# Kernel tuning notes

Measured on AMD Instinct MI355X. Metric: run time of the kernel, lower is better.

## Reference

```python
import jax, jax.numpy as jnp
import numpy as np

N_NODES = 100000


def gcn_conv(x, row, col, norm, W, b):
    # PyG GCNConv: linear transform first, then normalized aggregation.
    h = x @ W                                   # [N, D_out]
    msg = h[col] * norm[:, None]                # gather sources, scale  [E', D_out]
    out = jax.ops.segment_sum(msg, row, num_segments=N_NODES)
    return out + b


def _build_norm(edge_index, n):
    # add self-loops
    loops = jnp.arange(n, dtype=edge_index.dtype)
    row = jnp.concatenate([edge_index[0], loops])  # targets
    col = jnp.concatenate([edge_index[1], loops])  # sources
    deg = jax.ops.segment_sum(jnp.ones(row.shape[0], jnp.float32), row, num_segments=n)
    dinv = jnp.where(deg > 0, jax.lax.rsqrt(deg), 0.0)
    norm = dinv[row] * dinv[col]
    return row, col, norm


def setup_inputs() -> dict:
    key = jax.random.key(0)
    k = jax.random.split(key, 5)
    N, E, IN, H, OUT = N_NODES, 1_600_000, 128, 64, 64
    x = jax.random.normal(k[0], (N, IN), jnp.float32)
    edge_index = jax.random.randint(k[1], (2, E), 0, N, dtype=jnp.int32)
    W1 = jax.random.normal(k[2], (IN, H), jnp.float32) / np.sqrt(IN)
    b1 = jnp.zeros((H,), jnp.float32)
    W2 = jax.random.normal(k[3], (H, OUT), jnp.float32) / np.sqrt(H)
    b2 = jnp.zeros((OUT,), jnp.float32)
    return {"x": x, "edge_index": edge_index, "W1": W1, "b1": b1, "W2": W2, "b2": b2}


def reference(x, edge_index, W1, b1, W2, b2):
    row, col, norm = _build_norm(edge_index, N_NODES)
    h = jax.nn.relu(gcn_conv(x, row, col, norm, W1, b1))
    # dropout is identity in eval mode
    out = gcn_conv(h, row, col, norm, W2, b2)
    return out
```

## Files before the change

### kernel.cpp

```cpp
#include <hip/hip_runtime.h>
#include <hip/hip_bf16.h>
#include <stdint.h>


#define BUCKET_CAP 64
#define GATHER_CAP 58
#define NB_SHIFT 8
#define BIN_W (1 << NB_SHIFT)
#define EPB 4096

typedef __bf16 bf16x8 __attribute__((ext_vector_type(8)));
typedef float  f32x4  __attribute__((ext_vector_type(4)));

__device__ __forceinline__ void prep_w_one(const float* __restrict__ W,
                                           __bf16* __restrict__ Wsw, int t) {
    int lane = t & 63;
    int f = t >> 6;
    int kt = f >> 2, nt = f & 3;
    int k0 = kt * 32 + ((lane >> 4) * 8);
    int n  = nt * 16 + (lane & 15);
    __bf16* dst = Wsw + (size_t)t * 8;
#pragma unroll
    for (int j = 0; j < 8; ++j)
        dst[j] = (__bf16)W[(size_t)(k0 + j) * 64 + n];
}

__global__ void k_binA_gemm1(const int* __restrict__ row, const int* __restrict__ col,
                             int E, int NB, int NBLK,
                             const float* __restrict__ W1, const float* __restrict__ W2,
                             __bf16* __restrict__ W2sw,
                             int* __restrict__ lofs_g, int* __restrict__ binbuf,
                             const float* __restrict__ X, __bf16* __restrict__ H1,
                             int n_mtiles) {
    __shared__ int hist[512];
    __shared__ int lofs[512];
    __shared__ int cur[512];
    __shared__ int stage[EPB];
    __shared__ int wsum[4];
    int t = threadIdx.x;
    int blk = blockIdx.x;

    if (blk >= NBLK + 2) {
        constexpr int KT = 4;
        constexpr int M_ITERS = 2;
        constexpr int KDIM = KT * 32;
        int lane = t & 63;
        int wave = t >> 6;
        int task = (blk - NBLK - 2) * 4 + wave;
        int mt0 = task * M_ITERS;

        bf16x8 Bf[KT * 4];
#pragma unroll
        for (int kt = 0; kt < KT; ++kt) {
#pragma unroll
            for (int nt = 0; nt < 4; ++nt) {
                int k0 = kt * 32 + ((lane >> 4) * 8);
                int n  = nt * 16 + (lane & 15);
                bf16x8 b;
#pragma unroll
                for (int j = 0; j < 8; ++j)
                    b[j] = (__bf16)W1[(size_t)(k0 + j) * 64 + n];
                Bf[kt * 4 + nt] = b;
            }
        }

        int m_in_tile = lane & 15;
        int k0 = (lane >> 4) * 8;

        for (int it = 0; it < M_ITERS; ++it) {
            int mt = mt0 + it;
            if (mt >= n_mtiles) return;
            int node = mt * 16 + m_in_tile;

            bf16x8 Af[KT];
#pragma unroll
            for (int kt = 0; kt < KT; ++kt) {
                const f32x4* p = (const f32x4*)(X + (size_t)node * KDIM + kt * 32 + k0);
                f32x4 lo = p[0], hi = p[1];
                bf16x8 a;
#pragma unroll
                for (int j = 0; j < 4; ++j) {
                    a[j]     = (__bf16)lo[j];
                    a[j + 4] = (__bf16)hi[j];
                }
                Af[kt] = a;
            }

#pragma unroll
            for (int nt = 0; nt < 4; ++nt) {
                f32x4 c = {0.f, 0.f, 0.f, 0.f};
#pragma unroll
                for (int kt = 0; kt < KT; ++kt)
                    c = __builtin_amdgcn_mfma_f32_16x16x32_bf16(Af[kt], Bf[kt * 4 + nt], c, 0, 0, 0);
                int nd = mt * 16 + (lane >> 4) * 4;
                int ft = nt * 16 + (lane & 15);
#pragma unroll
                for (int r = 0; r < 4; ++r)
                    H1[(size_t)(nd + r) * 64 + ft] = (__bf16)c[r];
            }
        }
        return;
    }

    if (blk >= NBLK) {
        int b = blk - NBLK;
        prep_w_one(W2, W2sw, b * 256 + t);
        return;
    }

    int e0 = blk * EPB;
    int nE = E - e0; if (nE > EPB) nE = EPB;

    for (int i = t; i < 512; i += 256) hist[i] = 0;
    __syncthreads();

    int rr[EPB / 256], cc[EPB / 256];
#pragma unroll
    for (int k = 0; k < EPB / 256; ++k) {
        int idx = k * 256 + t;
        if (idx < nE) {
            rr[k] = row[e0 + idx];
            cc[k] = col[e0 + idx];
            atomicAdd(&hist[((unsigned)rr[k]) >> NB_SHIFT], 1);
        } else rr[k] = -1;
    }
    __syncthreads();

    int h0 = hist[2 * t], h1 = hist[2 * t + 1];
    int s = h0 + h1;
    int v = s;
#pragma unroll
    for (int off = 1; off < 64; off <<= 1) {
        int u = __shfl_up(v, off);
        if ((t & 63) >= off) v += u;
    }
    if ((t & 63) == 63) wsum[t >> 6] = v;
    __syncthreads();
    int wo = 0;
    for (int w = 0; w < (t >> 6); ++w) wo += wsum[w];
    int base = v + wo - s;
    lofs[2 * t]     = base;
    lofs[2 * t + 1] = base + h0;
    cur[2 * t]      = base;
    cur[2 * t + 1]  = base + h0;
    __syncthreads();

#pragma unroll
    for (int k = 0; k < EPB / 256; ++k) {
        if (rr[k] >= 0) {
            int b = ((unsigned)rr[k]) >> NB_SHIFT;
            int p = atomicAdd(&cur[b], 1);
            stage[p] = (cc[k] << NB_SHIFT) | (rr[k] & (BIN_W - 1));
        }
    }
    __syncthreads();

    for (int i = t; i < nE; i += 256)
        binbuf[(size_t)blk * EPB + i] = stage[i];
    for (int i = t; i <= NB; i += 256)
        lofs_g[(size_t)blk * (NB + 1) + i] = lofs[i];
}

#define BB_THREADS 512
__global__ __launch_bounds__(512, 2)
void k_binB(const int* __restrict__ lofs_g, const int* __restrict__ binbuf,
            int NBLK, int NB, int* __restrict__ cnt, float* __restrict__ dinv,
            int* __restrict__ bucket, int N) {
    __shared__ int loc[BIN_W];
    __shared__ int S0[400];
    __shared__ int S1[400];
    int t = threadIdx.x;
    int k = blockIdx.x;
    int lane = t & 63;
    int wave = t >> 6;
    int node0 = k << NB_SHIFT;

    for (int i = t; i < BIN_W; i += BB_THREADS) loc[i] = 0;
    for (int i = t; i < NBLK; i += BB_THREADS) {
        S0[i] = lofs_g[(size_t)i * (NB + 1) + k];
        S1[i] = lofs_g[(size_t)i * (NB + 1) + k + 1];
    }
    __syncthreads();

    {
        int sub = lane >> 4;
        int li  = lane & 15;
        for (int sbase = wave * 4; sbase < NBLK; sbase += 32) {
            int seg = sbase + sub;
            if (seg < NBLK) {
                int s0 = S0[seg], s1 = S1[seg];
                const int* __restrict__ segp = binbuf + (size_t)seg * EPB;
                for (int j = s0 + li; j < s1; j += 16) {
                    int v = segp[j];
                    int rl = v & (BIN_W - 1);
                    int c  = (int)(((unsigned)v) >> NB_SHIFT);
                    int p = atomicAdd(&loc[rl], 1);
                    if (p < BUCKET_CAP)
                        bucket[(size_t)(node0 + rl) * BUCKET_CAP + p] = c;
                }
            }
        }
    }
    __syncthreads();

    int node = node0 + t;
    if (t < BIN_W && node < N) {
        int d = loc[t];
        cnt[node] = d;
        dinv[node] = rsqrtf((float)(d + 1));
    }
}

__device__ __forceinline__ float tree_reduce8(const float acc8[8], int lane) {
    bool b2 = (lane & 32) != 0;
    float a4[4];
#pragma unroll
    for (int i = 0; i < 4; ++i) {
        float send = b2 ? acc8[i] : acc8[i + 4];
        float keep = b2 ? acc8[i + 4] : acc8[i];
        a4[i] = keep + __shfl_xor(send, 32);
    }
    bool b1 = (lane & 16) != 0;
    float a2[2];
#pragma unroll
    for (int i = 0; i < 2; ++i) {
        float s2 = b1 ? a4[i] : a4[i + 2];
        float k2 = b1 ? a4[i + 2] : a4[i];
        a2[i] = k2 + __shfl_xor(s2, 16);
    }
    bool b0 = (lane & 8) != 0;
    float s1 = b0 ? a2[0] : a2[1];
    float k1 = b0 ? a2[1] : a2[0];
    return k1 + __shfl_xor(s1, 8);
}

__device__ __forceinline__ void gather_pair_wide(const __bf16* __restrict__ H,
                                                 const int* __restrict__ cnt,
                                                 const float* __restrict__ dinv,
                                                 const int* __restrict__ bucket,
                                                 int na, int nb, int lane,
                                                 float& sa, float& sb,
                                                 float& dia, float& dib) {
    int dega = cnt[na], degb = cnt[nb];
    int ma = dega > GATHER_CAP ? GATHER_CAP : dega;
    int mb = degb > GATHER_CAP ? GATHER_CAP : degb;
    int   cja = (lane < ma) ? bucket[(size_t)na * BUCKET_CAP + lane] : na;
    int   cjb = (lane < mb) ? bucket[(size_t)nb * BUCKET_CAP + lane] : nb;
    float dja = (lane <= ma) ? dinv[cja] : 0.f;
    float djb = (lane <= mb) ? dinv[cjb] : 0.f;
    dia = dinv[na];
    dib = dinv[nb];

    int r = lane >> 3, g = lane & 7;
    const __bf16* __restrict__ Hg = H + g * 8;
    float aa[8] = {0.f, 0.f, 0.f, 0.f, 0.f, 0.f, 0.f, 0.f};
    float ab[8] = {0.f, 0.f, 0.f, 0.f, 0.f, 0.f, 0.f, 0.f};
    int mpa = ma + 1, mpb = mb + 1;

    if (mpa <= 16 && mpb <= 16) {
        bf16x8 La[2], Lb[2];
#pragma unroll
        for (int u = 0; u < 2; ++u) {
            int ca = __shfl(cja, u * 8 + r);
            int cb = __shfl(cjb, u * 8 + r);
            La[u] = *(const bf16x8*)(Hg + (size_t)ca * 64);
            Lb[u] = *(const bf16x8*)(Hg + (size_t)cb * 64);
        }
#pragma unroll
        for (int u = 0; u < 2; ++u) {
            float da = __shfl(dja, u * 8 + r);
            float db = __shfl(djb, u * 8 + r);
#pragma unroll
            for (int i = 0; i < 8; ++i) {
                aa[i] = fmaf(da, (float)La[u][i], aa[i]);
                ab[i] = fmaf(db, (float)Lb[u][i], ab[i]);
            }
        }
    } else if (mpa <= 24 && mpb <= 24) {
        bf16x8 La[3], Lb[3];
#pragma unroll
        for (int u = 0; u < 3; ++u) {
            int ca = __shfl(cja, u * 8 + r);
            int cb = __shfl(cjb, u * 8 + r);
            La[u] = *(const bf16x8*)(Hg + (size_t)ca * 64);
            Lb[u] = *(const bf16x8*)(Hg + (size_t)cb * 64);
        }
#pragma unroll
        for (int u = 0; u < 3; ++u) {
            float da = __shfl(dja, u * 8 + r);
            float db = __shfl(djb, u * 8 + r);
#pragma unroll
            for (int i = 0; i < 8; ++i) {
                aa[i] = fmaf(da, (float)La[u][i], aa[i]);
                ab[i] = fmaf(db, (float)Lb[u][i], ab[i]);
            }
        }
    } else {
        bf16x8 La[4], Lb[4];
#pragma unroll
        for (int u = 0; u < 4; ++u) {
            int ca = __shfl(cja, u * 8 + r);
            int cb = __shfl(cjb, u * 8 + r);
            La[u] = *(const bf16x8*)(Hg + (size_t)ca * 64);
            Lb[u] = *(const bf16x8*)(Hg + (size_t)cb * 64);
        }
#pragma unroll
        for (int u = 0; u < 4; ++u) {
            float da = __shfl(dja, u * 8 + r);
            float db = __shfl(djb, u * 8 + r);
#pragma unroll
            for (int i = 0; i < 8; ++i) {
                aa[i] = fmaf(da, (float)La[u][i], aa[i]);
                ab[i] = fmaf(db, (float)Lb[u][i], ab[i]);
            }
        }
        if (mpa > 32) {
#pragma unroll 1
            for (int j = 32; j < mpa; j += 8) {
                int   c = __shfl(cja, j + r);
                float d = __shfl(dja, j + r);
                bf16x8 h = *(const bf16x8*)(Hg + (size_t)c * 64);
#pragma unroll
                for (int i = 0; i < 8; ++i)
                    aa[i] = fmaf(d, (float)h[i], aa[i]);
            }
        }
        if (mpb > 32) {
#pragma unroll 1
            for (int j = 32; j < mpb; j += 8) {
                int   c = __shfl(cjb, j + r);
                float d = __shfl(djb, j + r);
                bf16x8 h = *(const bf16x8*)(Hg + (size_t)c * 64);
#pragma unroll
                for (int i = 0; i < 8; ++i)
                    ab[i] = fmaf(d, (float)h[i], ab[i]);
            }
        }
    }

    sa = tree_reduce8(aa, lane);
    sb = tree_reduce8(ab, lane);
}

__global__ __launch_bounds__(256, 4)
void k_agg1_gemm2(const __bf16* __restrict__ H1, const int* __restrict__ cnt,
                  const float* __restrict__ dinv,
                  const int* __restrict__ bucket, const float* __restrict__ b1,
                  const __bf16* __restrict__ W2sw,
                  __bf16* __restrict__ H2, int N) {
    __shared__ __bf16 G1s[16][72];
    int lane = threadIdx.x & 63;
    int wave = threadIdx.x >> 6;
    int node0 = blockIdx.x * 16;
    int f = (lane & 7) * 8 + (lane >> 3);
    float bias = b1[f];

#pragma unroll
    for (int i = 0; i < 4; i += 2) {
        int nrow = wave * 4 + i;
        int na = node0 + nrow;
        int nb = na + 1;
        int nac = na < N ? na : 0;
        int nbc = nb < N ? nb : 0;
        float sa, sb, dia, dib;
        gather_pair_wide(H1, cnt, dinv, bucket, nac, nbc, lane, sa, sb, dia, dib);
        float va = fmaxf(fmaf(dia, sa, bias), 0.f);
        float vb = fmaxf(fmaf(dib, sb, bias), 0.f);
        if (na >= N) va = 0.f;
        if (nb >= N) vb = 0.f;
        G1s[nrow][f]     = (__bf16)va;
        G1s[nrow + 1][f] = (__bf16)vb;
    }
    __syncthreads();

    int m = lane & 15;
    int k0 = (lane >> 4) * 8;
    const bf16x8* Wv = (const bf16x8*)W2sw;
    bf16x8 Bf0 = Wv[(size_t)(0 * 4 + wave) * 64 + lane];
    bf16x8 Bf1 = Wv[(size_t)(1 * 4 + wave) * 64 + lane];
    bf16x8 Af0 = *(const bf16x8*)&G1s[m][k0];
    bf16x8 Af1 = *(const bf16x8*)&G1s[m][32 + k0];

    f32x4 c = {0.f, 0.f, 0.f, 0.f};
    c = __builtin_amdgcn_mfma_f32_16x16x32_bf16(Af0, Bf0, c, 0, 0, 0);
    c = __builtin_amdgcn_mfma_f32_16x16x32_bf16(Af1, Bf1, c, 0, 0, 0);

    int nd = node0 + (lane >> 4) * 4;
    int ft = wave * 16 + (lane & 15);
#pragma unroll
    for (int r = 0; r < 4; ++r)
        if (nd + r < N)
            H2[(size_t)(nd + r) * 64 + ft] = (__bf16)c[r];
}

__global__ __launch_bounds__(256, 4)
void k_agg2(const __bf16* __restrict__ H2, const int* __restrict__ cnt,
            const float* __restrict__ dinv,
            const int* __restrict__ bucket, const float* __restrict__ b2,
            float* __restrict__ out, int N) {
    int wave = threadIdx.x >> 6;
    int lane = threadIdx.x & 63;
    int na = blockIdx.x * 8 + wave * 2;
    if (na >= N) return;
    int nb = na + 1;
    int nbc = nb < N ? nb : 0;
    int f = (lane & 7) * 8 + (lane >> 3);
    float sa, sb, dia, dib;
    gather_pair_wide(H2, cnt, dinv, bucket, na, nbc, lane, sa, sb, dia, dib);
    float bias = b2[f];
    out[(size_t)na * 64 + f] = fmaf(dia, sa, bias);
    if (nb < N)
        out[(size_t)nb * 64 + f] = fmaf(dib, sb, bias);
}

extern "C" void kernel_launch(void* const* d_in, const int* in_sizes, int n_in,
                              void* d_out, int out_size, void* d_ws, size_t ws_size,
                              hipStream_t stream) {
    (void)n_in; (void)out_size; (void)ws_size;
    const float* x  = (const float*)d_in[0];
    const int*   ei = (const int*)d_in[1];
    const float* W1 = (const float*)d_in[2];
    const float* b1 = (const float*)d_in[3];
    const float* W2 = (const float*)d_in[4];
    const float* b2 = (const float*)d_in[5];

    const int N = in_sizes[0] / 128;
    const int E = in_sizes[1] / 2;
    const int* row = ei;
    const int* col = ei + E;

    const int NB   = (N + BIN_W - 1) >> NB_SHIFT;
    const int NBLK = (E + EPB - 1) / EPB;

    char* ws = (char*)d_ws;
    size_t off = 0;
    auto take = [&](size_t bytes) -> char* {
        char* p = ws + off;
        off += (bytes + 255) & ~(size_t)255;
        return p;
    };
    int*    cnt    = (int*)   take((size_t)N * 4);
    float*  dinv   = (float*) take((size_t)N * 4);
    int*    lofs_g = (int*)   take((size_t)NBLK * (NB + 1) * 4);
    int*    bucket = (int*)   take((size_t)N * BUCKET_CAP * 4);
    __bf16* W2sw   = (__bf16*)take((size_t)8  * 64 * 8 * 2);
    __bf16* H1     = (__bf16*)take((size_t)N * 64 * 2);
    size_t h2_bytes  = (size_t)N * 64 * 2;
    size_t bin_bytes = (size_t)NBLK * EPB * 4;
    char*   unionbuf = take(h2_bytes > bin_bytes ? h2_bytes : bin_bytes);
    int*    binbuf = (int*)unionbuf;
    __bf16* H2     = (__bf16*)unionbuf;

    const int n_mtiles = (N + 15) / 16;
    const int GB1 = (n_mtiles / 2 + 1 + 3) / 4;

    k_binA_gemm1<<<NBLK + 2 + GB1, 256, 0, stream>>>(row, col, E, NB, NBLK,
                                                     W1, W2, W2sw,
                                                     lofs_g, binbuf, x, H1, n_mtiles);
    k_binB<<<NB, BB_THREADS, 0, stream>>>(lofs_g, binbuf, NBLK, NB,
                                          cnt, dinv, bucket, N);
    k_agg1_gemm2<<<(N + 15) / 16, 256, 0, stream>>>(H1, cnt, dinv, bucket, b1, W2sw, H2, N);
    k_agg2<<<(N + 7) / 8, 256, 0, stream>>>(H2, cnt, dinv, bucket, b2, (float*)d_out, N);
}
```

Before: 203.0 us.

## Pre-scale features by source dinv to drop dependent dinv gathers in aggregation

Folds the source-side normalization dinv[col] into the feature rows ahead of time. H1 rows are scaled in place at the end of k_binB, and H2 is scaled at store time in the gemm2 epilogue. The gather loop then uses 0/1 weights instead of a dependent random load of dinv[cja] per neighbor, and the bucket load is issued unconditionally so it can overlap with the degree load. The cost is an extra read-modify-write pass over H1 in k_binB and an additional bf16 rounding of the scaled features.

```diff
diff --git a/kernel.cpp b/kernel.cpp
--- a/kernel.cpp
+++ b/kernel.cpp
@@ -165,7 +165,7 @@
 __global__ __launch_bounds__(512, 2)
 void k_binB(const int* __restrict__ lofs_g, const int* __restrict__ binbuf,
             int NBLK, int NB, int* __restrict__ cnt, float* __restrict__ dinv,
-            int* __restrict__ bucket, int N) {
+            int* __restrict__ bucket, __bf16* __restrict__ H1, int N) {
     __shared__ int loc[BIN_W];
     __shared__ int S0[400];
     __shared__ int S1[400];
@@ -209,6 +209,20 @@
         cnt[node] = d;
         dinv[node] = rsqrtf((float)(d + 1));
     }
+
+    for (int idx = t; idx < BIN_W * 8; idx += BB_THREADS) {
+        int nl = idx >> 3;
+        int n2 = node0 + nl;
+        if (n2 < N) {
+            float dv = rsqrtf((float)(loc[nl] + 1));
+            bf16x8* p = (bf16x8*)(H1 + (size_t)n2 * 64 + (idx & 7) * 8);
+            bf16x8 vv = *p;
+            bf16x8 o;
+#pragma unroll
+            for (int j = 0; j < 8; ++j) o[j] = (__bf16)(dv * (float)vv[j]);
+            *p = o;
+        }
+    }
 }
 
 __device__ __forceinline__ float tree_reduce8(const float acc8[8], int lane) {
@@ -238,18 +252,20 @@
                                                  const int* __restrict__ cnt,
                                                  const float* __restrict__ dinv,
                                                  const int* __restrict__ bucket,
-                                                 int na, int nb, int lane,
+                                                 int na, int nb, int lane, int N,
                                                  float& sa, float& sb,
                                                  float& dia, float& dib) {
     int dega = cnt[na], degb = cnt[nb];
+    int rawa = bucket[(size_t)na * BUCKET_CAP + lane];
+    int rawb = bucket[(size_t)nb * BUCKET_CAP + lane];
+    dia = dinv[na];
+    dib = dinv[nb];
     int ma = dega > GATHER_CAP ? GATHER_CAP : dega;
     int mb = degb > GATHER_CAP ? GATHER_CAP : degb;
-    int   cja = (lane < ma) ? bucket[(size_t)na * BUCKET_CAP + lane] : na;
-    int   cjb = (lane < mb) ? bucket[(size_t)nb * BUCKET_CAP + lane] : nb;
-    float dja = (lane <= ma) ? dinv[cja] : 0.f;
-    float djb = (lane <= mb) ? dinv[cjb] : 0.f;
-    dia = dinv[na];
-    dib = dinv[nb];
+    int cja = (lane < ma && (unsigned)rawa < (unsigned)N) ? rawa : na;
+    int cjb = (lane < mb && (unsigned)rawb < (unsigned)N) ? rawb : nb;
+    float wja = (lane <= ma) ? 1.f : 0.f;
+    float wjb = (lane <= mb) ? 1.f : 0.f;
 
     int r = lane >> 3, g = lane & 7;
     const __bf16* __restrict__ Hg = H + g * 8;
@@ -268,8 +284,8 @@
         }
 #pragma unroll
         for (int u = 0; u < 2; ++u) {
-            float da = __shfl(dja, u * 8 + r);
-            float db = __shfl(djb, u * 8 + r);
+            float da = __shfl(wja, u * 8 + r);
+            float db = __shfl(wjb, u * 8 + r);
 #pragma unroll
             for (int i = 0; i < 8; ++i) {
                 aa[i] = fmaf(da, (float)La[u][i], aa[i]);
@@ -287,8 +303,8 @@
         }
 #pragma unroll
         for (int u = 0; u < 3; ++u) {
-            float da = __shfl(dja, u * 8 + r);
-            float db = __shfl(djb, u * 8 + r);
+            float da = __shfl(wja, u * 8 + r);
+            float db = __shfl(wjb, u * 8 + r);
 #pragma unroll
             for (int i = 0; i < 8; ++i) {
                 aa[i] = fmaf(da, (float)La[u][i], aa[i]);
@@ -306,8 +322,8 @@
         }
 #pragma unroll
         for (int u = 0; u < 4; ++u) {
-            float da = __shfl(dja, u * 8 + r);
-            float db = __shfl(djb, u * 8 + r);
+            float da = __shfl(wja, u * 8 + r);
+            float db = __shfl(wjb, u * 8 + r);
 #pragma unroll
             for (int i = 0; i < 8; ++i) {
                 aa[i] = fmaf(da, (float)La[u][i], aa[i]);
@@ -318,7 +334,7 @@
 #pragma unroll 1
             for (int j = 32; j < mpa; j += 8) {
                 int   c = __shfl(cja, j + r);
-                float d = __shfl(dja, j + r);
+                float d = __shfl(wja, j + r);
                 bf16x8 h = *(const bf16x8*)(Hg + (size_t)c * 64);
 #pragma unroll
                 for (int i = 0; i < 8; ++i)
@@ -329,7 +345,7 @@
 #pragma unroll 1
             for (int j = 32; j < mpb; j += 8) {
                 int   c = __shfl(cjb, j + r);
-                float d = __shfl(djb, j + r);
+                float d = __shfl(wjb, j + r);
                 bf16x8 h = *(const bf16x8*)(Hg + (size_t)c * 64);
 #pragma unroll
                 for (int i = 0; i < 8; ++i)
@@ -363,7 +379,7 @@
         int nac = na < N ? na : 0;
         int nbc = nb < N ? nb : 0;
         float sa, sb, dia, dib;
-        gather_pair_wide(H1, cnt, dinv, bucket, nac, nbc, lane, sa, sb, dia, dib);
+        gather_pair_wide(H1, cnt, dinv, bucket, nac, nbc, lane, N, sa, sb, dia, dib);
         float va = fmaxf(fmaf(dia, sa, bias), 0.f);
         float vb = fmaxf(fmaf(dib, sb, bias), 0.f);
         if (na >= N) va = 0.f;
@@ -390,7 +406,7 @@
 #pragma unroll
     for (int r = 0; r < 4; ++r)
         if (nd + r < N)
-            H2[(size_t)(nd + r) * 64 + ft] = (__bf16)c[r];
+            H2[(size_t)(nd + r) * 64 + ft] = (__bf16)(dinv[nd + r] * c[r]);
 }
 
 __global__ __launch_bounds__(256, 4)
@@ -406,7 +422,7 @@
     int nbc = nb < N ? nb : 0;
     int f = (lane & 7) * 8 + (lane >> 3);
     float sa, sb, dia, dib;
-    gather_pair_wide(H2, cnt, dinv, bucket, na, nbc, lane, sa, sb, dia, dib);
+    gather_pair_wide(H2, cnt, dinv, bucket, na, nbc, lane, N, sa, sb, dia, dib);
     float bias = b2[f];
     out[(size_t)na * 64 + f] = fmaf(dia, sa, bias);
     if (nb < N)
@@ -458,7 +474,7 @@
                                                      W1, W2, W2sw,
                                                      lofs_g, binbuf, x, H1, n_mtiles);
     k_binB<<<NB, BB_THREADS, 0, stream>>>(lofs_g, binbuf, NBLK, NB,
-                                          cnt, dinv, bucket, N);
+                                          cnt, dinv, bucket, H1, N);
     k_agg1_gemm2<<<(N + 15) / 16, 256, 0, stream>>>(H1, cnt, dinv, bucket, b1, W2sw, H2, N);
     k_agg2<<<(N + 7) / 8, 256, 0, stream>>>(H2, cnt, dinv, bucket, b2, (float*)d_out, N);
 }
```

After: 199.3 us. About the same (-1.8%).
